# Performance work log

Hardware: AMD Instinct MI355X
Metric: run time of the kernel (lower is better)

## Reference

```python
import jax, jax.numpy as jnp
import numpy as np

K_NN = 2       # module k: number of nearest neighbors used for mean kNN distance
ALPHA = 1.1    # threshold = mean + alpha * std


def setup_inputs() -> dict:
    key = jax.random.key(0)
    x = jax.random.normal(key, (16, 4096, 3), dtype=jnp.float32)
    return {"x": x}


def reference(x):
    # x: [B, K, 3] point cloud
    # pairwise squared distances: ||xi||^2 - 2 xi.xj + ||xj||^2  -> [B, K, K]
    inner = -2.0 * jnp.einsum("bkd,bjd->bkj", x, x)
    xx = jnp.sum(x * x, axis=-1)                       # [B, K]
    dist = xx[:, :, None] + inner + xx[:, None, :]     # [B, K, K]

    # k+1 smallest distances (includes self-distance 0), drop self
    neg_value, _ = jax.lax.top_k(-dist, K_NN + 1)      # [B, K, k+1]
    value = -neg_value[..., 1:]                        # [B, K, k] kNN distances
    value = jnp.mean(value, axis=-1)                   # [B, K] mean kNN distance

    mean = jnp.mean(value, axis=-1)                    # [B]
    std = jnp.std(value, axis=-1, ddof=1)              # [B] unbiased, like torch.std
    threshold = mean + ALPHA * std                     # [B]
    bool_mask = value <= threshold[:, None]            # [B, K]

    # Original returns a ragged list x[i][mask[i]]; for fixed shapes under jit we
    # return the points with outliers zeroed plus the boolean keep-mask, which
    # carries identical information.
    sel_pc = jnp.where(bool_mask[..., None], x, jnp.zeros((), x.dtype))  # [B, K, 3]
    return sel_pc, bool_mask
```

## Files before the change

kernel.cpp:

```cpp
#include <hip/hip_runtime.h>
#include <math.h>

#define B_SZ 16
#define K_PTS 4096
#define ALPHA 1.1f

#define JS 16
#define JTT (K_PTS / JS)
#define ICH 1024
#define THR 256

#define BIGF 3.0e38f

__device__ __forceinline__ void insert2(float d, float& m0, float& m1) {
    m1 = __builtin_amdgcn_fmed3f(d, m0, m1);
    m0 = fminf(d, m0);
}
__device__ __forceinline__ void insert3(float d, float& m0, float& m1, float& m2) {
    m2 = __builtin_amdgcn_fmed3f(d, m1, m2);
    m1 = __builtin_amdgcn_fmed3f(d, m0, m1);
    m0 = fminf(d, m0);
}

__global__ __launch_bounds__(256) void sor_partial2(
    const float* __restrict__ x, float* __restrict__ ws)
{
    __shared__ float4 pts[JTT];
    const int b  = blockIdx.y;
    const int ic = blockIdx.x >> 4;
    const int js = blockIdx.x & 15;
    const int j0 = js * JTT;
    const float* xb = x + (size_t)b * K_PTS * 3;

    for (int p = threadIdx.x; p < JTT; p += THR) {
        float a0 = xb[(j0 + p) * 3 + 0];
        float a1 = xb[(j0 + p) * 3 + 1];
        float a2 = xb[(j0 + p) * 3 + 2];
        pts[p] = make_float4(a0, a1, a2, a0 * a0 + a1 * a1 + a2 * a2);
    }
    __syncthreads();

    const int ibase = ic * ICH + threadIdx.x;
    const bool diag = ((js >> 2) == ic);
    const int kstar = js & 3;

    int idx[4];
    #pragma unroll
    for (int c = 0; c < 4; ++c) idx[c] = ibase + c * THR;
    if (diag) { idx[0] = ibase + kstar * THR; idx[kstar] = ibase; }

    float x2[4], y2[4], z2[4], m0[4], m1[4];
    #pragma unroll
    for (int c = 0; c < 4; ++c) {
        const float* p = xb + (size_t)idx[c] * 3;
        x2[c] = -2.0f * p[0];
        y2[c] = -2.0f * p[1];
        z2[c] = -2.0f * p[2];
        m0[c] = BIGF; m1[c] = BIGF;
    }

    float* wbase = ws + (size_t)((b * JS + js) * 2) * K_PTS;

    if (diag) {
        float m2_0 = BIGF;
        #pragma unroll 8
        for (int j = 0; j < JTT; ++j) {
            const float4 pj = pts[j];
            {
                float t = fmaf(z2[0], pj.z, pj.w);
                t = fmaf(y2[0], pj.y, t);
                float d = fmaf(x2[0], pj.x, t);
                insert3(d, m0[0], m1[0], m2_0);
            }
            #pragma unroll
            for (int c = 1; c < 4; ++c) {
                float t = fmaf(z2[c], pj.z, pj.w);
                t = fmaf(y2[c], pj.y, t);
                float d = fmaf(x2[c], pj.x, t);
                insert2(d, m0[c], m1[c]);
            }
        }
        wbase[idx[0]]         = m1[0];
        wbase[K_PTS + idx[0]] = m2_0;
        #pragma unroll
        for (int c = 1; c < 4; ++c) {
            wbase[idx[c]]         = m0[c];
            wbase[K_PTS + idx[c]] = m1[c];
        }
    } else {
        #pragma unroll 8
        for (int j = 0; j < JTT; ++j) {
            const float4 pj = pts[j];
            #pragma unroll
            for (int c = 0; c < 4; ++c) {
                float t = fmaf(z2[c], pj.z, pj.w);
                t = fmaf(y2[c], pj.y, t);
                float d = fmaf(x2[c], pj.x, t);
                insert2(d, m0[c], m1[c]);
            }
        }
        #pragma unroll
        for (int c = 0; c < 4; ++c) {
            wbase[idx[c]]         = m0[c];
            wbase[K_PTS + idx[c]] = m1[c];
        }
    }
}

__global__ __launch_bounds__(256) void sor_merge(
    const float* __restrict__ x, const float* __restrict__ ws,
    float* __restrict__ value)
{
    const int gid = blockIdx.x * 256 + threadIdx.x;
    const int b = gid >> 12;
    const int i = gid & (K_PTS - 1);

    float m0 = BIGF, m1 = BIGF;
    #pragma unroll
    for (int js = 0; js < JS; ++js) {
        const float* w = ws + (size_t)((b * JS + js) * 2) * K_PTS + i;
        insert2(w[0], m0, m1);
        insert2(w[K_PTS], m0, m1);
    }
    const float a0 = x[(size_t)gid * 3 + 0];
    const float a1 = x[(size_t)gid * 3 + 1];
    const float a2 = x[(size_t)gid * 3 + 2];
    const float xx = a0 * a0 + a1 * a1 + a2 * a2;
    value[gid] = ((m0 + xx) + (m1 + xx)) * 0.5f;
}

__global__ __launch_bounds__(1024) void sor_mask_kernel(
    const float* __restrict__ x, float* __restrict__ out)
{
    const int b = blockIdx.x;
    const int tid = threadIdx.x;
    float* value = out + (size_t)B_SZ * K_PTS * 3;
    float* selpc = out;

    __shared__ float red[16];
    __shared__ float sh_mean, sh_thr;

    float v[4];
    float s = 0.0f;
    #pragma unroll
    for (int k = 0; k < 4; ++k) {
        v[k] = value[b * K_PTS + tid + k * 1024];
        s += v[k];
    }
    #pragma unroll
    for (int off = 32; off > 0; off >>= 1) s += __shfl_down(s, off, 64);
    if ((tid & 63) == 0) red[tid >> 6] = s;
    __syncthreads();
    if (tid == 0) {
        float t = 0.0f;
        for (int w = 0; w < 16; ++w) t += red[w];
        sh_mean = t * (1.0f / (float)K_PTS);
    }
    __syncthreads();
    const float mean = sh_mean;

    float q = 0.0f;
    #pragma unroll
    for (int k = 0; k < 4; ++k) { float dv = v[k] - mean; q += dv * dv; }
    #pragma unroll
    for (int off = 32; off > 0; off >>= 1) q += __shfl_down(q, off, 64);
    if ((tid & 63) == 0) red[tid >> 6] = q;
    __syncthreads();
    if (tid == 0) {
        float t = 0.0f;
        for (int w = 0; w < 16; ++w) t += red[w];
        sh_thr = mean + ALPHA * sqrtf(t / (float)(K_PTS - 1));
    }
    __syncthreads();
    const float thr = sh_thr;

    #pragma unroll
    for (int k = 0; k < 4; ++k) {
        const int i = tid + k * 1024;
        const bool keep = v[k] <= thr;
        value[b * K_PTS + i] = keep ? 1.0f : 0.0f;
        const size_t base = ((size_t)b * K_PTS + i) * 3;
        float x0 = x[base + 0];
        float x1 = x[base + 1];
        float x2 = x[base + 2];
        selpc[base + 0] = keep ? x0 : 0.0f;
        selpc[base + 1] = keep ? x1 : 0.0f;
        selpc[base + 2] = keep ? x2 : 0.0f;
    }
}

__global__ __launch_bounds__(256) void sor_value_kernel(
    const float* __restrict__ x, float* __restrict__ value)
{
    __shared__ float4 pts[K_PTS];
    const int b = blockIdx.y;
    const float* xb = x + (size_t)b * K_PTS * 3;
    for (int p = threadIdx.x; p < K_PTS; p += 256) {
        float a0 = xb[p * 3 + 0];
        float a1 = xb[p * 3 + 1];
        float a2 = xb[p * 3 + 2];
        pts[p] = make_float4(a0, a1, a2, a0 * a0 + a1 * a1 + a2 * a2);
    }
    __syncthreads();
    const int i = blockIdx.x * 256 + threadIdx.x;
    const float4 pi = pts[i];
    float m0 = BIGF, m1 = BIGF, m2 = BIGF;
    #pragma unroll 8
    for (int j = 0; j < K_PTS; ++j) {
        float4 pj = pts[j];
        float dot = pi.x * pj.x + pi.y * pj.y + pi.z * pj.z;
        float d = (pi.w - 2.0f * dot) + pj.w;
        insert3(d, m0, m1, m2);
    }
    value[b * K_PTS + i] = 0.5f * (m1 + m2);
}

extern "C" void kernel_launch(void* const* d_in, const int* in_sizes, int n_in,
                              void* d_out, int out_size, void* d_ws, size_t ws_size,
                              hipStream_t stream)
{
    const float* x = (const float*)d_in[0];
    float* out = (float*)d_out;
    float* value = out + (size_t)B_SZ * K_PTS * 3;

    const size_t ws_needed = (size_t)B_SZ * JS * 2 * K_PTS * sizeof(float);

    if (ws_size >= ws_needed) {
        float* ws = (float*)d_ws;
        dim3 gA((K_PTS / ICH) * JS, B_SZ);
        sor_partial2<<<gA, THR, 0, stream>>>(x, ws);
        sor_merge<<<(B_SZ * K_PTS) / 256, 256, 0, stream>>>(x, ws, value);
    } else {
        dim3 g1(K_PTS / 256, B_SZ);
        sor_value_kernel<<<g1, 256, 0, stream>>>(x, value);
    }
    sor_mask_kernel<<<B_SZ, 1024, 0, stream>>>(x, out);
}
```

Before: 45.33 us.

## Give each partial-kNN block all query points with 512 threads

The partial kNN kernel now has each block of 512 threads handle all 4096 query points (8 per thread) against one 256-point j-slice. Previously there were four i-chunks of 4 points per thread, each reloading the slice. Self-distance is handled per thread through a uniform insert3 slot, which removes the diag/non-diag branch. This raises register reuse of each shared-memory load and cuts redundant slice staging. It also shrinks the grid from 1024 to 256 blocks, lowering parallelism on a large GPU and raising register pressure.

```diff
diff --git a/kernel.cpp b/kernel.cpp
--- a/kernel.cpp
+++ b/kernel.cpp
@@ -7,8 +7,8 @@
 
 #define JS 16
 #define JTT (K_PTS / JS)
-#define ICH 1024
-#define THR 256
+#define THR 512
+#define NCH 8
 
 #define BIGF 3.0e38f
 
@@ -22,13 +22,12 @@
     m0 = fminf(d, m0);
 }
 
-__global__ __launch_bounds__(256) void sor_partial2(
+__global__ __launch_bounds__(THR) void sor_partial2(
     const float* __restrict__ x, float* __restrict__ ws)
 {
     __shared__ float4 pts[JTT];
     const int b  = blockIdx.y;
-    const int ic = blockIdx.x >> 4;
-    const int js = blockIdx.x & 15;
+    const int js = blockIdx.x;
     const int j0 = js * JTT;
     const float* xb = x + (size_t)b * K_PTS * 3;
 
@@ -40,70 +39,59 @@
     }
     __syncthreads();
 
-    const int ibase = ic * ICH + threadIdx.x;
-    const bool diag = ((js >> 2) == ic);
-    const int kstar = js & 3;
-
-    int idx[4];
-    #pragma unroll
-    for (int c = 0; c < 4; ++c) idx[c] = ibase + c * THR;
-    if (diag) { idx[0] = ibase + kstar * THR; idx[kstar] = ibase; }
-
-    float x2[4], y2[4], z2[4], m0[4], m1[4];
-    #pragma unroll
-    for (int c = 0; c < 4; ++c) {
+    const int tid = threadIdx.x;
+    const int cstar = js >> 1;
+    const bool has_self = ((tid >> 8) == (js & 1));
+
+    int idx[NCH];
+    #pragma unroll
+    for (int c = 0; c < NCH; ++c) {
+        int p = tid + c * THR;
+        if (c == 0) p = has_self ? (tid + cstar * THR) : tid;
+        else        p = (has_self && (c == cstar)) ? tid : p;
+        idx[c] = p;
+    }
+
+    float x2[NCH], y2[NCH], z2[NCH], m0[NCH], m1[NCH];
+    #pragma unroll
+    for (int c = 0; c < NCH; ++c) {
         const float* p = xb + (size_t)idx[c] * 3;
         x2[c] = -2.0f * p[0];
         y2[c] = -2.0f * p[1];
         z2[c] = -2.0f * p[2];
         m0[c] = BIGF; m1[c] = BIGF;
     }
-
-    float* wbase = ws + (size_t)((b * JS + js) * 2) * K_PTS;
-
-    if (diag) {
-        float m2_0 = BIGF;
-        #pragma unroll 8
-        for (int j = 0; j < JTT; ++j) {
-            const float4 pj = pts[j];
-            {
-                float t = fmaf(z2[0], pj.z, pj.w);
-                t = fmaf(y2[0], pj.y, t);
-                float d = fmaf(x2[0], pj.x, t);
-                insert3(d, m0[0], m1[0], m2_0);
-            }
-            #pragma unroll
-            for (int c = 1; c < 4; ++c) {
-                float t = fmaf(z2[c], pj.z, pj.w);
-                t = fmaf(y2[c], pj.y, t);
-                float d = fmaf(x2[c], pj.x, t);
-                insert2(d, m0[c], m1[c]);
-            }
-        }
-        wbase[idx[0]]         = m1[0];
-        wbase[K_PTS + idx[0]] = m2_0;
-        #pragma unroll
-        for (int c = 1; c < 4; ++c) {
-            wbase[idx[c]]         = m0[c];
-            wbase[K_PTS + idx[c]] = m1[c];
-        }
-    } else {
-        #pragma unroll 8
-        for (int j = 0; j < JTT; ++j) {
-            const float4 pj = pts[j];
-            #pragma unroll
-            for (int c = 0; c < 4; ++c) {
-                float t = fmaf(z2[c], pj.z, pj.w);
-                t = fmaf(y2[c], pj.y, t);
-                float d = fmaf(x2[c], pj.x, t);
-                insert2(d, m0[c], m1[c]);
-            }
+    float m2_0 = BIGF;
+
+    #pragma unroll 4
+    for (int j = 0; j < JTT; ++j) {
+        const float4 pj = pts[j];
+        {
+            float t = fmaf(z2[0], pj.z, pj.w);
+            t = fmaf(y2[0], pj.y, t);
+            float d = fmaf(x2[0], pj.x, t);
+            insert3(d, m0[0], m1[0], m2_0);
         }
         #pragma unroll
-        for (int c = 0; c < 4; ++c) {
-            wbase[idx[c]]         = m0[c];
-            wbase[K_PTS + idx[c]] = m1[c];
+        for (int c = 1; c < NCH; ++c) {
+            float t = fmaf(z2[c], pj.z, pj.w);
+            t = fmaf(y2[c], pj.y, t);
+            float d = fmaf(x2[c], pj.x, t);
+            insert2(d, m0[c], m1[c]);
         }
+    }
+
+    float* wbase = ws + (size_t)((b * JS + js) * 2) * K_PTS;
+    {
+        const float s0 = has_self ? m1[0] : m0[0];
+        const float s1 = has_self ? m2_0  : m1[0];
+        wbase[idx[0]]         = s0;
+        wbase[K_PTS + idx[0]] = s1;
+    }
+    #pragma unroll
+    for (int c = 1; c < NCH; ++c) {
+        wbase[idx[c]]         = m0[c];
+        wbase[K_PTS + idx[c]] = m1[c];
     }
 }
 
@@ -227,7 +215,7 @@
 
     if (ws_size >= ws_needed) {
         float* ws = (float*)d_ws;
-        dim3 gA((K_PTS / ICH) * JS, B_SZ);
+        dim3 gA(JS, B_SZ);
         sor_partial2<<<gA, THR, 0, stream>>>(x, ws);
         sor_merge<<<(B_SZ * K_PTS) / 256, 256, 0, stream>>>(x, ws, value);
     } else {
```

After: 46.07 us. Within noise of the previous version (+1.6%).
